# Performance work log

Measured on AMD Instinct MI355X. Metric: run time of the kernel, lower is better.

Reference implementation:

```python
import jax, jax.numpy as jnp
import numpy as np

B, H, E, DFF, K = 4096, 1024, 8, 4096, 2
THRESH = 0.1


def setup_inputs() -> dict:
    key = jax.random.key(0)
    ks = jax.random.split(key, 8)
    g = lambda k, shape, scale: (jax.random.normal(k, shape, jnp.float32) * scale)
    return {
        "x": jax.random.normal(ks[0], (B, H), jnp.float32),
        "gate_w1": g(ks[1], (H, H // 2), 0.03),
        "gate_b1": jnp.zeros((H // 2,), jnp.float32),
        "gate_w2": g(ks[2], (H // 2, E), 0.06),
        "gate_b2": jnp.zeros((E,), jnp.float32),
        "exp_w1": g(ks[3], (E, H, DFF), 0.03),
        "exp_b1": jnp.zeros((E, DFF), jnp.float32),
        "exp_w2": g(ks[4], (E, DFF, H), 0.015),
        "exp_b2": jnp.zeros((E, H), jnp.float32),
        "proj_w": g(ks[5], (E, H, H), 0.03),
        "blend": jnp.asarray(0.0, jnp.float32),
    }


def reference(x, gate_w1, gate_b1, gate_w2, gate_b2,
              exp_w1, exp_b1, exp_w2, exp_b2, proj_w, blend):
    # PathGate: Linear -> SiLU -> Linear, logits (B, E)
    logits = jax.nn.silu(x @ gate_w1 + gate_b1) @ gate_w2 + gate_b2
    # eval mode (training=False): plain softmax (Markov bayes adjustment = 0)
    gate_weights = jax.nn.softmax(logits, axis=-1)

    # top-k selection with firing threshold
    top_vals, top_idx = jax.lax.top_k(gate_weights, K)        # (B, K)
    keep = top_vals > THRESH                                  # (B, K)
    # scatter kept top-k weights back to dense (B, E) dispatch weights
    onehot = jax.nn.one_hot(top_idx, E, dtype=gate_weights.dtype)  # (B, K, E)
    w_full = jnp.sum(jnp.where(keep[..., None], top_vals[..., None], 0.0) * onehot, axis=1)  # (B, E)

    # per-expert MLP + out_proj, weighted combine (loop over fixed E experts)
    combined = jnp.zeros_like(x)
    for e in range(E):
        h = jax.nn.silu(x @ exp_w1[e] + exp_b1[e]) @ exp_w2[e] + exp_b2[e]  # (B, H)
        combined = combined + w_full[:, e:e + 1] * (h @ proj_w[e])

    total_weight = jnp.sum(w_full, axis=-1)                   # (B,)
    fired = total_weight > 0
    safe_tw = jnp.where(fired, total_weight, 1.0)
    combined = jnp.where(fired[:, None], combined / safe_tw[:, None], x)

    alpha = jax.nn.sigmoid(blend)
    output = alpha * combined + (1.0 - alpha) * x
    return output, gate_weights
```

## Files before the change

kernel.cpp:

```cpp
#include <hip/hip_runtime.h>
#include <hip/hip_bf16.h>
#include <cmath>

constexpr int NB = 4096;
constexpr int NH = 1024;
constexpr int NE = 8;
constexpr int NF = 4096;
constexpr int NG = 512;
constexpr float THRESH = 0.1f;
constexpr int PAD_ROWS = 128;
constexpr size_t MAXS = (size_t)2 * NB;
constexpr size_t ROWS = MAXS + PAD_ROWS;


typedef float  f32x4  __attribute__((ext_vector_type(4)));
typedef __bf16 bf16x8 __attribute__((ext_vector_type(8)));
typedef __bf16 bf16x4 __attribute__((ext_vector_type(4)));

typedef __attribute__((address_space(1))) void gvoid_t;
typedef __attribute__((address_space(3))) void svoid_t;

__device__ __forceinline__ void gl_lds16(const void* g, void* l)
{
    __builtin_amdgcn_global_load_lds((gvoid_t*)g, (svoid_t*)l, 16, 0, 0);
}

__device__ __forceinline__ float silu_f(float v) { return v / (1.f + expf(-v)); }

__global__ void k_sentinel(float* out, float code)
{
    if (threadIdx.x == 0 && blockIdx.x == 0) out[0] = code;
}

__global__ __launch_bounds__(256) void k_tconv(
    const float* __restrict__ in, __bf16* __restrict__ out, int R, int C)
{
    __shared__ float t[64][65];
    const int e = blockIdx.z;
    const float* I = in + (size_t)e * R * C;
    __bf16* O = out + (size_t)e * R * C;
    const int r0 = blockIdx.y * 64, c0 = blockIdx.x * 64;
    const int tid = threadIdx.x;
#pragma unroll
    for (int i = 0; i < 16; i++) {
        int idx = tid + i * 256;
        int r = idx >> 6, c = idx & 63;
        t[r][c] = I[(size_t)(r0 + r) * C + c0 + c];
    }
    __syncthreads();
#pragma unroll
    for (int i = 0; i < 16; i++) {
        int idx = tid + i * 256;
        int c = idx >> 6, r = idx & 63;
        O[(size_t)(c0 + c) * R + r0 + r] = (__bf16)t[r][c];
    }
}

__global__ __launch_bounds__(256) void k_gate(
    const float* __restrict__ x, const float* __restrict__ w1,
    const float* __restrict__ b1, float* __restrict__ hidden)
{
    __shared__ float As[16][68];
    __shared__ float Bs[16][64];
    const int tid = threadIdx.x;
    const int r0 = blockIdx.y * 64, c0 = blockIdx.x * 64;
    const int tx = tid & 15, ty = tid >> 4;
    float acc[4][4] = {};
    for (int k0 = 0; k0 < NH; k0 += 16) {
#pragma unroll
        for (int i = 0; i < 4; i++) {
            int e = tid + i * 256;
            int m = e >> 4, kk = e & 15;
            As[kk][m] = x[(size_t)(r0 + m) * NH + k0 + kk];
        }
#pragma unroll
        for (int i = 0; i < 4; i++) {
            int e = tid + i * 256;
            int kk = e >> 6, n = e & 63;
            Bs[kk][n] = w1[(size_t)(k0 + kk) * NG + c0 + n];
        }
        __syncthreads();
#pragma unroll
        for (int kk = 0; kk < 16; kk++) {
            f32x4 a = *(const f32x4*)&As[kk][ty * 4];
            f32x4 b = *(const f32x4*)&Bs[kk][tx * 4];
#pragma unroll
            for (int i = 0; i < 4; i++)
#pragma unroll
                for (int j = 0; j < 4; j++)
                    acc[i][j] = fmaf(a[i], b[j], acc[i][j]);
        }
        __syncthreads();
    }
#pragma unroll
    for (int i = 0; i < 4; i++) {
        int row = r0 + ty * 4 + i;
        f32x4 o;
#pragma unroll
        for (int j = 0; j < 4; j++)
            o[j] = silu_f(acc[i][j] + b1[c0 + tx * 4 + j]);
        *(f32x4*)&hidden[(size_t)row * NG + c0 + tx * 4] = o;
    }
}

__global__ __launch_bounds__(64) void k_router(
    const float* __restrict__ hidden, const float* __restrict__ w2,
    const float* __restrict__ b2, float* __restrict__ gw_out,
    int* __restrict__ count, int* __restrict__ slot_row,
    float* __restrict__ slot_w, float* __restrict__ row_total,
    int* __restrict__ row_fired)
{
    const int r = blockIdx.x;
    const int l = threadIdx.x;
    float pe[NE] = {};
    for (int k = l; k < NG; k += 64) {
        float h = hidden[(size_t)r * NG + k];
        const float* wr = w2 + (size_t)k * NE;
#pragma unroll
        for (int e = 0; e < NE; e++) pe[e] += h * wr[e];
    }
#pragma unroll
    for (int e = 0; e < NE; e++) {
#pragma unroll
        for (int m = 1; m < 64; m <<= 1) pe[e] += __shfl_xor(pe[e], m);
    }
    float logit[NE];
    float mx = -1e30f;
#pragma unroll
    for (int e = 0; e < NE; e++) { logit[e] = pe[e] + b2[e]; mx = fmaxf(mx, logit[e]); }
    float w[NE], s = 0.f;
#pragma unroll
    for (int e = 0; e < NE; e++) { w[e] = expf(logit[e] - mx); s += w[e]; }
    float inv = 1.f / s;
#pragma unroll
    for (int e = 0; e < NE; e++) w[e] *= inv;
    if (l < NE) gw_out[(size_t)r * NE + l] = w[l];

    int i1 = 0; float v1 = w[0];
#pragma unroll
    for (int e = 1; e < NE; e++) if (w[e] > v1) { v1 = w[e]; i1 = e; }
    int i2 = -1; float v2 = -1.f;
#pragma unroll
    for (int e = 0; e < NE; e++) if (e != i1 && w[e] > v2) { v2 = w[e]; i2 = e; }

    bool k1 = v1 > THRESH, k2 = v2 > THRESH;
    float total = (k1 ? v1 : 0.f) + (k2 ? v2 : 0.f);
    if (l == 0) {
        row_total[r] = total;
        row_fired[r] = (total > 0.f) ? 1 : 0;
        if (k1) { int p = atomicAdd(&count[i1], 1); slot_row[i1 * NB + p] = r; slot_w[i1 * NB + p] = v1; }
        if (k2) { int p = atomicAdd(&count[i2], 1); slot_row[i2 * NB + p] = r; slot_w[i2 * NB + p] = v2; }
    }
}

__global__ void k_offsets(const int* __restrict__ count, int* __restrict__ offs)
{
    if (threadIdx.x == 0 && blockIdx.x == 0) {
        int s = 0;
        for (int e = 0; e < NE; e++) { offs[e] = s; s += count[e]; }
    }
}

__global__ __launch_bounds__(256) void k_xc(
    const float* __restrict__ x, const int* __restrict__ count,
    const int* __restrict__ offs, const int* __restrict__ slot_row,
    __bf16* __restrict__ Xc)
{
    const int s = blockIdx.x;
    int e = 0;
#pragma unroll
    for (int i = 1; i < NE; i++) if (s >= offs[i]) e = i;
    if (s >= offs[NE - 1] + count[NE - 1]) return;
    const int r = slot_row[e * NB + (s - offs[e])];
    const float* src = x + (size_t)r * NH;
    __bf16* dst = Xc + (size_t)s * NH;
    const int t = threadIdx.x;
    f32x4 v = *(const f32x4*)(src + t * 4);
    bf16x4 o;
#pragma unroll
    for (int j = 0; j < 4; j++) o[j] = (__bf16)v[j];
    *(bf16x4*)(dst + t * 4) = o;
}

template<int ACT, int OM>
__global__ __launch_bounds__(256) void k_gemm2(
    const __bf16* __restrict__ A, int lda,
    const __bf16* __restrict__ Wt, size_t wstride,
    const float* __restrict__ bias, int bstride,
    __bf16* __restrict__ outB, float* __restrict__ outF,
    int N, int Kd, int X,
    const int* __restrict__ count, const int* __restrict__ offs,
    const int* __restrict__ slot_row, const float* __restrict__ slot_w)
{
    const int Y = gridDim.y;
    const int flat = blockIdx.y * gridDim.x + blockIdx.x;
    const int grp  = flat / (8 * Y);
    const int rem  = flat - grp * 8 * Y;
    const int p    = grp * 8 + (rem & 7);
    const int yy   = rem >> 3;
    const int e  = p / X;
    const int n0 = (p % X) * 128;
    const int cnt = count[e];
    const int row0 = yy * 128;
    if (row0 >= cnt) return;
    const int off = offs[e];
    const __bf16* W = Wt + (size_t)e * wstride;
    const int tid = threadIdx.x;
    const int lane = tid & 63, wid = tid >> 6;
    const int wm = (wid >> 1) * 64, wn = (wid & 1) * 64;
    const int arow0 = off + row0;

    __shared__ __align__(16) unsigned char sA[16384];
    __shared__ __align__(16) unsigned char sB[16384];

    f32x4 acc[4][4];
#pragma unroll
    for (int mi = 0; mi < 4; mi++)
#pragma unroll
        for (int ni = 0; ni < 4; ni++)
            acc[mi][ni] = (f32x4){0.f, 0.f, 0.f, 0.f};

    const int sub = lane >> 3;
    const int kcx = (lane & 7) ^ sub;

    for (int k0 = 0; k0 < Kd; k0 += 64) {
#pragma unroll
        for (int i = 0; i < 4; i++) {
            int c = wid * 4 + i;
            int row = c * 8 + sub;
            gl_lds16(A + (size_t)(arow0 + row) * lda + k0 + kcx * 8,
                     sA + c * 1024 + lane * 16);
        }
#pragma unroll
        for (int i = 0; i < 4; i++) {
            int c = wid * 4 + i;
            int n = c * 8 + sub;
            gl_lds16(W + (size_t)(n0 + n) * Kd + k0 + kcx * 8,
                     sB + c * 1024 + lane * 16);
        }
        __syncthreads();
#pragma unroll
        for (int ks = 0; ks < 2; ks++) {
            bf16x8 af[4], bfr[4];
            const int kb = ks * 64 + ((lane >> 4) << 4);
#pragma unroll
            for (int mi = 0; mi < 4; mi++) {
                int row = wm + mi * 16 + (lane & 15);
                af[mi] = *(const bf16x8*)(sA + row * 128 + (kb ^ ((row & 7) << 4)));
            }
#pragma unroll
            for (int ni = 0; ni < 4; ni++) {
                int row = wn + ni * 16 + (lane & 15);
                bfr[ni] = *(const bf16x8*)(sB + row * 128 + (kb ^ ((row & 7) << 4)));
            }
#pragma unroll
            for (int mi = 0; mi < 4; mi++)
#pragma unroll
                for (int ni = 0; ni < 4; ni++)
                    acc[mi][ni] = __builtin_amdgcn_mfma_f32_16x16x32_bf16(
                        af[mi], bfr[ni], acc[mi][ni], 0, 0, 0);
        }
        __syncthreads();
    }

    const int q = lane >> 4, cl = lane & 15;
#pragma unroll
    for (int mi = 0; mi < 4; mi++) {
#pragma unroll
        for (int r = 0; r < 4; r++) {
            int srow = row0 + wm + mi * 16 + q * 4 + r;
            if (srow >= cnt) continue;
            if (OM == 0) {
#pragma unroll
                for (int ni = 0; ni < 4; ni++) {
                    int col = n0 + wn + ni * 16 + cl;
                    float vv = acc[mi][ni][r] + bias[(size_t)e * bstride + col];
                    if (ACT) vv = silu_f(vv);
                    outB[(size_t)(off + srow) * N + col] = (__bf16)vv;
                }
            } else {
                int grow = slot_row[e * NB + srow];
                float wsl = slot_w[e * NB + srow];
#pragma unroll
                for (int ni = 0; ni < 4; ni++) {
                    int col = n0 + wn + ni * 16 + cl;
                    atomicAdd(&outF[(size_t)grow * NH + col], wsl * acc[mi][ni][r]);
                }
            }
        }
    }
}

__global__ __launch_bounds__(256) void k_final(
    const float* __restrict__ x,
    const float* __restrict__ row_total, const int* __restrict__ row_fired,
    const float* __restrict__ blend, float* __restrict__ out)
{
    int idx = blockIdx.x * 256 + threadIdx.x;
    int r = idx >> 8;
    int c = (idx & 255) << 2;
    float alpha = 1.f / (1.f + expf(-blend[0]));
    f32x4 cb = *(const f32x4*)(out + (size_t)r * NH + c);
    f32x4 xv = *(const f32x4*)(x + (size_t)r * NH + c);
    int fired = row_fired[r];
    float inv_t = fired ? (1.f / row_total[r]) : 0.f;
    f32x4 o;
#pragma unroll
    for (int j = 0; j < 4; j++)
        o[j] = fired ? (alpha * (cb[j] * inv_t) + (1.f - alpha) * xv[j]) : xv[j];
    *(f32x4*)&out[(size_t)r * NH + c] = o;
}

extern "C" void kernel_launch(void* const* d_in, const int* in_sizes, int n_in,
                              void* d_out, int out_size, void* d_ws, size_t ws_size,
                              hipStream_t stream)
{
    float* out_main = (float*)d_out;
    float* gw_out   = (float*)d_out + (size_t)NB * NH;

    static const long long EXP[11] = {
        (long long)NB * NH, (long long)NH * NG, NG, (long long)NG * NE, NE,
        (long long)NE * NH * NF, (long long)NE * NF,
        (long long)NE * NF * NH, (long long)NE * NH,
        (long long)NE * NH * NH, 1
    };
    bool ok = (n_in == 11);
    if (ok)
        for (int i = 0; i < 11; i++)
            if ((long long)in_sizes[i] != EXP[i]) { ok = false; break; }
    if (!ok) {
        k_sentinel<<<1, 1, 0, stream>>>((float*)d_out, 2000.f + n_in);
        return;
    }

    const float* x    = (const float*)d_in[0];
    const float* gw1  = (const float*)d_in[1];
    const float* gb1  = (const float*)d_in[2];
    const float* gw2  = (const float*)d_in[3];
    const float* gb2  = (const float*)d_in[4];
    const float* ew1  = (const float*)d_in[5];
    const float* eb1  = (const float*)d_in[6];
    const float* ew2  = (const float*)d_in[7];
    const float* eb2  = (const float*)d_in[8];
    const float* pw   = (const float*)d_in[9];
    const float* blnd = (const float*)d_in[10];

    size_t need = 0;
    size_t off_meta   = need;   need += 512;
    size_t off_srow   = need;   need += (size_t)NE * NB * 4;
    size_t off_sw     = need;   need += (size_t)NE * NB * 4;
    size_t off_total  = need;   need += (size_t)NB * 4;
    size_t off_fired  = need;   need += (size_t)NB * 4;
    size_t off_hidden = need;   need += (size_t)NB * NG * 4;
    size_t a_xc  = need;
    size_t a_h1  = a_xc + ROWS * NH * 2;
    size_t a_h2  = a_h1 + ROWS * NF * 2;
    size_t a_w1  = a_h2 + ROWS * NH * 2;
    size_t a_w2  = a_w1 + (size_t)NE * NH * NF * 2;
    size_t a_wp  = a_w2 + (size_t)NE * NF * NH * 2;
    size_t need_A = a_wp + (size_t)NE * NH * NH * 2;

    char* ws = (char*)d_ws;
    int*   count     = (int*)(ws + off_meta);
    int*   offs      = count + 8;
    int*   slot_row  = (int*)(ws + off_srow);
    float* slot_w    = (float*)(ws + off_sw);
    float* row_total = (float*)(ws + off_total);
    int*   row_fired = (int*)(ws + off_fired);
    float* hidden    = (float*)(ws + off_hidden);

    if (ws_size < need_A) {
        k_sentinel<<<1, 1, 0, stream>>>((float*)d_out,
                                        1000.f + (float)(ws_size >> 20));
        return;
    }
    __bf16* Xc  = (__bf16*)(ws + a_xc);
    __bf16* H1  = (__bf16*)(ws + a_h1);
    __bf16* H2  = (__bf16*)(ws + a_h2);
    __bf16* Wt1 = (__bf16*)(ws + a_w1);
    __bf16* Wt2 = (__bf16*)(ws + a_w2);
    __bf16* Wtp = (__bf16*)(ws + a_wp);

    hipMemsetAsync(count, 0, 512, stream);
    hipMemsetAsync(out_main, 0, (size_t)NB * NH * 4, stream);

    k_gate<<<dim3(NG / 64, NB / 64), 256, 0, stream>>>(x, gw1, gb1, hidden);
    k_router<<<dim3(NB), 64, 0, stream>>>(hidden, gw2, gb2, gw_out,
                                          count, slot_row, slot_w, row_total, row_fired);
    k_offsets<<<1, 1, 0, stream>>>(count, offs);

    k_tconv<<<dim3(NF / 64, NH / 64, NE), 256, 0, stream>>>(ew1, Wt1, NH, NF);
    k_tconv<<<dim3(NH / 64, NF / 64, NE), 256, 0, stream>>>(ew2, Wt2, NF, NH);
    k_tconv<<<dim3(NH / 64, NH / 64, NE), 256, 0, stream>>>(pw,  Wtp, NH, NH);
    k_xc<<<dim3((int)MAXS), 256, 0, stream>>>(x, count, offs, slot_row, Xc);

    k_gemm2<1, 0><<<dim3(32 * NE, NB / 128), 256, 0, stream>>>(
        Xc, NH, Wt1, (size_t)NH * NF, eb1, NF,
        H1, nullptr, NF, NH, 32, count, offs, slot_row, slot_w);
    k_gemm2<0, 0><<<dim3(8 * NE, NB / 128), 256, 0, stream>>>(
        H1, NF, Wt2, (size_t)NF * NH, eb2, NH,
        H2, nullptr, NH, NF, 8, count, offs, slot_row, slot_w);
    k_gemm2<0, 1><<<dim3(8 * NE, NB / 128), 256, 0, stream>>>(
        H2, NH, Wtp, (size_t)NH * NH, eb2 , 0,
        nullptr, out_main, NH, NH, 8, count, offs, slot_row, slot_w);

    k_final<<<dim3(NB * NH / 1024), 256, 0, stream>>>(x, row_total,
                                                      row_fired, blnd, out_main);
}
```

Baseline: 586.6 us.

## Merge gate GEMM and weight transposes into one prework kernel

Combines the gate first-layer GEMM and the three fp32-to-bf16 expert weight transpose kernels into a single launch that dispatches on block index, so the small gate GEMM overlaps with the bandwidth-bound transposes. The transpose store path is rewritten to write 4 bf16 values per thread as a vector instead of scalar stores. The grouped block swizzle in the expert GEMM is removed in favour of direct blockIdx mapping, which may reduce L2 reuse of weight tiles.

```diff
diff --git a/kernel.cpp b/kernel.cpp
--- a/kernel.cpp
+++ b/kernel.cpp
@@ -32,74 +32,105 @@
     if (threadIdx.x == 0 && blockIdx.x == 0) out[0] = code;
 }
 
-__global__ __launch_bounds__(256) void k_tconv(
-    const float* __restrict__ in, __bf16* __restrict__ out, int R, int C)
-{
-    __shared__ float t[64][65];
-    const int e = blockIdx.z;
-    const float* I = in + (size_t)e * R * C;
-    __bf16* O = out + (size_t)e * R * C;
-    const int r0 = blockIdx.y * 64, c0 = blockIdx.x * 64;
+__device__ __forceinline__ void tconv_body(
+    const float* __restrict__ I, __bf16* __restrict__ O, int R, int C,
+    int bx, int by, float* smem)
+{
+    const int r0 = by * 64, c0 = bx * 64;
     const int tid = threadIdx.x;
 #pragma unroll
     for (int i = 0; i < 16; i++) {
         int idx = tid + i * 256;
         int r = idx >> 6, c = idx & 63;
-        t[r][c] = I[(size_t)(r0 + r) * C + c0 + c];
+        smem[r * 65 + c] = I[(size_t)(r0 + r) * C + c0 + c];
     }
     __syncthreads();
-#pragma unroll
-    for (int i = 0; i < 16; i++) {
-        int idx = tid + i * 256;
-        int c = idx >> 6, r = idx & 63;
-        O[(size_t)(c0 + c) * R + r0 + r] = (__bf16)t[r][c];
-    }
-}
-
-__global__ __launch_bounds__(256) void k_gate(
-    const float* __restrict__ x, const float* __restrict__ w1,
-    const float* __restrict__ b1, float* __restrict__ hidden)
-{
-    __shared__ float As[16][68];
-    __shared__ float Bs[16][64];
-    const int tid = threadIdx.x;
-    const int r0 = blockIdx.y * 64, c0 = blockIdx.x * 64;
-    const int tx = tid & 15, ty = tid >> 4;
-    float acc[4][4] = {};
-    for (int k0 = 0; k0 < NH; k0 += 16) {
+    const int cl = tid >> 4;
+    const int rq = tid & 15;
+#pragma unroll
+    for (int i = 0; i < 4; i++) {
+        int c = cl + i * 16;
+        bf16x4 v;
+#pragma unroll
+        for (int j = 0; j < 4; j++)
+            v[j] = (__bf16)smem[(rq * 4 + j) * 65 + c];
+        *(bf16x4*)&O[(size_t)(c0 + c) * R + r0 + rq * 4] = v;
+    }
+}
+
+__global__ __launch_bounds__(256) void k_prework(
+    const float* __restrict__ x, const float* __restrict__ gw1,
+    const float* __restrict__ gb1, float* __restrict__ hidden,
+    const float* __restrict__ ew1, __bf16* __restrict__ Wt1,
+    const float* __restrict__ ew2, __bf16* __restrict__ Wt2,
+    const float* __restrict__ pw,  __bf16* __restrict__ Wtp)
+{
+    __shared__ float smem[64 * 65];
+    int id = blockIdx.x;
+
+    if (id < 512) {
+        float* As = smem;
+        float* Bs = smem + 16 * 68;
+        const int tid = threadIdx.x;
+        const int r0 = (id >> 3) * 64, c0 = (id & 7) * 64;
+        const int tx = tid & 15, ty = tid >> 4;
+        float acc[4][4] = {};
+        for (int k0 = 0; k0 < NH; k0 += 16) {
+#pragma unroll
+            for (int i = 0; i < 4; i++) {
+                int e = tid + i * 256;
+                int m = e >> 4, kk = e & 15;
+                As[kk * 68 + m] = x[(size_t)(r0 + m) * NH + k0 + kk];
+            }
+#pragma unroll
+            for (int i = 0; i < 4; i++) {
+                int e = tid + i * 256;
+                int kk = e >> 6, n = e & 63;
+                Bs[kk * 64 + n] = gw1[(size_t)(k0 + kk) * NG + c0 + n];
+            }
+            __syncthreads();
+#pragma unroll
+            for (int kk = 0; kk < 16; kk++) {
+                f32x4 a = *(const f32x4*)&As[kk * 68 + ty * 4];
+                f32x4 b = *(const f32x4*)&Bs[kk * 64 + tx * 4];
+#pragma unroll
+                for (int i = 0; i < 4; i++)
+#pragma unroll
+                    for (int j = 0; j < 4; j++)
+                        acc[i][j] = fmaf(a[i], b[j], acc[i][j]);
+            }
+            __syncthreads();
+        }
 #pragma unroll
         for (int i = 0; i < 4; i++) {
-            int e = tid + i * 256;
-            int m = e >> 4, kk = e & 15;
-            As[kk][m] = x[(size_t)(r0 + m) * NH + k0 + kk];
-        }
-#pragma unroll
-        for (int i = 0; i < 4; i++) {
-            int e = tid + i * 256;
-            int kk = e >> 6, n = e & 63;
-            Bs[kk][n] = w1[(size_t)(k0 + kk) * NG + c0 + n];
-        }
-        __syncthreads();
-#pragma unroll
-        for (int kk = 0; kk < 16; kk++) {
-            f32x4 a = *(const f32x4*)&As[kk][ty * 4];
-            f32x4 b = *(const f32x4*)&Bs[kk][tx * 4];
-#pragma unroll
-            for (int i = 0; i < 4; i++)
-#pragma unroll
-                for (int j = 0; j < 4; j++)
-                    acc[i][j] = fmaf(a[i], b[j], acc[i][j]);
-        }
-        __syncthreads();
-    }
-#pragma unroll
-    for (int i = 0; i < 4; i++) {
-        int row = r0 + ty * 4 + i;
-        f32x4 o;
-#pragma unroll
-        for (int j = 0; j < 4; j++)
-            o[j] = silu_f(acc[i][j] + b1[c0 + tx * 4 + j]);
-        *(f32x4*)&hidden[(size_t)row * NG + c0 + tx * 4] = o;
+            int row = r0 + ty * 4 + i;
+            f32x4 o;
+#pragma unroll
+            for (int j = 0; j < 4; j++)
+                o[j] = silu_f(acc[i][j] + gb1[c0 + tx * 4 + j]);
+            *(f32x4*)&hidden[(size_t)row * NG + c0 + tx * 4] = o;
+        }
+        return;
+    }
+    id -= 512;
+    if (id < 8192) {
+        int bx = id & 63, by = (id >> 6) & 15, e = id >> 10;
+        tconv_body(ew1 + (size_t)e * NH * NF, Wt1 + (size_t)e * NH * NF,
+                   NH, NF, bx, by, smem);
+        return;
+    }
+    id -= 8192;
+    if (id < 8192) {
+        int bx = id & 15, by = (id >> 4) & 63, e = id >> 10;
+        tconv_body(ew2 + (size_t)e * NF * NH, Wt2 + (size_t)e * NF * NH,
+                   NF, NH, bx, by, smem);
+        return;
+    }
+    id -= 8192;
+    {
+        int bx = id & 15, by = (id >> 4) & 15, e = id >> 8;
+        tconv_body(pw + (size_t)e * NH * NH, Wtp + (size_t)e * NH * NH,
+                   NH, NH, bx, by, smem);
     }
 }
 
@@ -192,16 +223,11 @@
     const int* __restrict__ count, const int* __restrict__ offs,
     const int* __restrict__ slot_row, const float* __restrict__ slot_w)
 {
-    const int Y = gridDim.y;
-    const int flat = blockIdx.y * gridDim.x + blockIdx.x;
-    const int grp  = flat / (8 * Y);
-    const int rem  = flat - grp * 8 * Y;
-    const int p    = grp * 8 + (rem & 7);
-    const int yy   = rem >> 3;
-    const int e  = p / X;
-    const int n0 = (p % X) * 128;
+    const int bx = blockIdx.x;
+    const int e  = bx / X;
+    const int n0 = (bx % X) * 128;
     const int cnt = count[e];
-    const int row0 = yy * 128;
+    const int row0 = blockIdx.y * 128;
     if (row0 >= cnt) return;
     const int off = offs[e];
     const __bf16* W = Wt + (size_t)e * wstride;
@@ -384,14 +410,12 @@
     hipMemsetAsync(count, 0, 512, stream);
     hipMemsetAsync(out_main, 0, (size_t)NB * NH * 4, stream);
 
-    k_gate<<<dim3(NG / 64, NB / 64), 256, 0, stream>>>(x, gw1, gb1, hidden);
+    k_prework<<<dim3(512 + 8192 + 8192 + 2048), 256, 0, stream>>>(
+        x, gw1, gb1, hidden, ew1, Wt1, ew2, Wt2, pw, Wtp);
+
     k_router<<<dim3(NB), 64, 0, stream>>>(hidden, gw2, gb2, gw_out,
                                           count, slot_row, slot_w, row_total, row_fired);
     k_offsets<<<1, 1, 0, stream>>>(count, offs);
-
-    k_tconv<<<dim3(NF / 64, NH / 64, NE), 256, 0, stream>>>(ew1, Wt1, NH, NF);
-    k_tconv<<<dim3(NH / 64, NF / 64, NE), 256, 0, stream>>>(ew2, Wt2, NF, NH);
-    k_tconv<<<dim3(NH / 64, NH / 64, NE), 256, 0, stream>>>(pw,  Wtp, NH, NH);
     k_xc<<<dim3((int)MAXS), 256, 0, stream>>>(x, count, offs, slot_row, Xc);
 
     k_gemm2<1, 0><<<dim3(32 * NE, NB / 128), 256, 0, stream>>>(
```

Result: faster. 542.4 us (-7.5%).
